# Optimization experiments

Hardware: AMD Instinct MI355X
Metric: run time of the kernel (lower is better)

The kernel has to match this reference:

```python
import jax, jax.numpy as jnp
import numpy as np

N = 50000
E = 800000
D_IN = 128
D_H = 128
N_CLASSES = 40
N_HIDDEN = 2


def _gcn_norm(edge_index, num_nodes):
    # Add self loops, compute symmetric normalization D^-1/2 (A+I) D^-1/2
    loops = jnp.arange(num_nodes, dtype=edge_index.dtype)
    src = jnp.concatenate([edge_index[0], loops])
    dst = jnp.concatenate([edge_index[1], loops])
    deg = jax.ops.segment_sum(jnp.ones_like(src, dtype=jnp.float32), dst,
                              num_segments=num_nodes)
    dinv = jnp.where(deg > 0, jax.lax.rsqrt(jnp.maximum(deg, 1.0)), 0.0)
    norm = dinv[src] * dinv[dst]  # [E+N]
    return src, dst, norm


def _gcn_conv(x, src, dst, norm, W, b):
    h = x @ W                          # [N, d_out] transform first (PyG order)
    msg = h[src] * norm[:, None]       # gather + scale, [E+N, d_out]
    out = jax.ops.segment_sum(msg, dst, num_segments=x.shape[0])
    return out + b


def setup_inputs() -> dict:
    key = jax.random.key(0)
    ks = jax.random.split(key, 8)
    x = jax.random.normal(ks[0], (N, D_IN), dtype=jnp.float32)
    edge_index = jax.random.randint(ks[1], (2, E), 0, N, dtype=jnp.int64)
    s = 1.0 / np.sqrt(D_IN)
    W1 = jax.random.uniform(ks[2], (D_IN, D_H), minval=-s, maxval=s, dtype=jnp.float32)
    b1 = jnp.zeros((D_H,), dtype=jnp.float32)
    sh = 1.0 / np.sqrt(D_H)
    Wh = jax.random.uniform(ks[3], (N_HIDDEN, D_H, D_H), minval=-sh, maxval=sh, dtype=jnp.float32)
    bh = jnp.zeros((N_HIDDEN, D_H), dtype=jnp.float32)
    Wf = jax.random.uniform(ks[4], (D_H, N_CLASSES), minval=-sh, maxval=sh, dtype=jnp.float32)
    bf = jnp.zeros((N_CLASSES,), dtype=jnp.float32)
    return {"x": x, "edge_index": edge_index, "W1": W1, "b1": b1,
            "Wh": Wh, "bh": bh, "Wf": Wf, "bf": bf}


def reference(x, edge_index, W1, b1, Wh, bh, Wf, bf):
    src, dst, norm = _gcn_norm(edge_index, x.shape[0])
    h = jax.nn.relu(_gcn_conv(x, src, dst, norm, W1, b1))
    for i in range(Wh.shape[0]):  # small fixed layer count
        h = jax.nn.relu(_gcn_conv(h, src, dst, norm, Wh[i], bh[i]))
    # extra relu in original forward is a no-op after relu above
    return h @ Wf + bf
```

## Files before the change

### kernel.cpp

```cpp
#include <hip/hip_runtime.h>

#define D 128
#define NC 40

typedef __attribute__((ext_vector_type(8))) short short8v;
typedef __attribute__((ext_vector_type(4))) float f32x4;

__device__ __forceinline__ unsigned short f2bf(float f) {
    unsigned u = __float_as_uint(f);
    u += 0x7fff + ((u >> 16) & 1);
    return (unsigned short)(u >> 16);
}
__device__ __forceinline__ float bf2f(unsigned short h) {
    return __uint_as_float(((unsigned)h) << 16);
}


__global__ void detect_kernel(const int* __restrict__ ei, int* __restrict__ flag) {
    __shared__ int any;
    if (threadIdx.x == 0) any = 0;
    __syncthreads();
    if (ei[threadIdx.x * 2 + 1] != 0) any = 1;
    __syncthreads();
    if (threadIdx.x == 0) *flag = (any == 0) ? 1 : 0;
}

__device__ __forceinline__ int load_idx(const int* ei, long long pos, int is64) {
    return is64 ? ei[pos * 2] : ei[pos];
}

__global__ void count_deg_kernel(const int* __restrict__ ei, const int* __restrict__ flag,
                                 int* __restrict__ deg, int E) {
    int e = blockIdx.x * blockDim.x + threadIdx.x;
    if (e >= E) return;
    int is64 = *flag;
    int d = load_idx(ei, (long long)E + e, is64);
    atomicAdd(&deg[d], 1);
}

__global__ void scan_kernel(const int* __restrict__ deg, int* __restrict__ rowptr,
                            int* __restrict__ fill, float* __restrict__ dinv, int n) {
    __shared__ int wsum[16];
    int t = threadIdx.x;
    int lane = t & 63, w = t >> 6;
    int base = 0;
    int nchunk = (n + 1023) >> 10;
    for (int c = 0; c < nchunk; ++c) {
        int i = (c << 10) + t;
        int v = (i < n) ? deg[i] : 0;
        int s = v;
        #pragma unroll
        for (int off = 1; off < 64; off <<= 1) {
            int x = __shfl_up(s, off, 64);
            if (lane >= off) s += x;
        }
        if (lane == 63) wsum[w] = s;
        __syncthreads();
        int wbase = 0, total = 0;
        #pragma unroll
        for (int j = 0; j < 16; ++j) {
            int ws_j = wsum[j];
            if (j < w) wbase += ws_j;
            total += ws_j;
        }
        int excl = wbase + s - v;
        if (i < n) {
            rowptr[i] = base + excl;
            fill[i]   = base + excl;
            dinv[i]   = rsqrtf((float)(v + 1));
        }
        __syncthreads();
        base += total;
    }
    if (t == 0) rowptr[n] = base;
}

__global__ void scatter_kernel(const int* __restrict__ ei, const int* __restrict__ flag,
                               int* __restrict__ fill, const float* __restrict__ dinv,
                               int2* __restrict__ col2, int E) {
    int e = blockIdx.x * blockDim.x + threadIdx.x;
    if (e >= E) return;
    int is64 = *flag;
    int s = load_idx(ei, (long long)e, is64);
    int d = load_idx(ei, (long long)E + e, is64);
    int pos = atomicAdd(&fill[d], 1);
    col2[pos] = make_int2(s, __float_as_int(dinv[s]));
}

__launch_bounds__(256)
__global__ void gemm128_mfma_kernel(const float* __restrict__ A, const float* __restrict__ W,
                                    float* __restrict__ C, int M) {
    __shared__ unsigned short Ah[64 * 128];
    __shared__ unsigned short Al[64 * 128];
    int t = threadIdx.x;
    int l = t & 63, w = t >> 6;
    int lr = l & 15, lh = l >> 4;

    short8v bhi[2][4], blo[2][4];
    int n0 = w * 32;
    #pragma unroll
    for (int ni = 0; ni < 2; ++ni) {
        #pragma unroll
        for (int ks = 0; ks < 4; ++ks) {
            int n = n0 + ni * 16 + lr;
            int kb = ks * 32 + lh * 8;
            #pragma unroll
            for (int j = 0; j < 8; ++j) {
                float wv = W[(kb + j) * 128 + n];
                unsigned short hi = f2bf(wv);
                unsigned short lo = f2bf(wv - bf2f(hi));
                bhi[ni][ks][j] = (short)hi;
                blo[ni][ks][j] = (short)lo;
            }
        }
    }

    int row0 = blockIdx.x * 64;
    #pragma unroll
    for (int c = 0; c < 4; ++c) {
        int chunk = c * 256 + t;
        int r  = chunk >> 4;
        int kc = chunk & 15;
        int gr = row0 + r; if (gr >= M) gr = M - 1;
        float4 a0 = *(const float4*)&A[(size_t)gr * 128 + kc * 8];
        float4 a1 = *(const float4*)&A[(size_t)gr * 128 + kc * 8 + 4];
        float av[8] = {a0.x, a0.y, a0.z, a0.w, a1.x, a1.y, a1.z, a1.w};
        short8v hv, lv;
        #pragma unroll
        for (int j = 0; j < 8; ++j) {
            unsigned short hi = f2bf(av[j]);
            hv[j] = (short)hi;
            lv[j] = (short)f2bf(av[j] - bf2f(hi));
        }
        int off = (r << 8) + ((kc << 4) ^ ((r & 7) << 4));
        *(short8v*)((char*)Ah + off) = hv;
        *(short8v*)((char*)Al + off) = lv;
    }
    __syncthreads();

    f32x4 acc[4][2];
    #pragma unroll
    for (int mi = 0; mi < 4; ++mi)
        #pragma unroll
        for (int ni = 0; ni < 2; ++ni)
            acc[mi][ni] = (f32x4){0.f, 0.f, 0.f, 0.f};

    #pragma unroll
    for (int mi = 0; mi < 4; ++mi) {
        int row = mi * 16 + lr;
        #pragma unroll
        for (int ks = 0; ks < 4; ++ks) {
            int off = (row << 8) + (((ks << 6) + (lh << 4)) ^ ((row & 7) << 4));
            short8v ah = *(short8v*)((char*)Ah + off);
            short8v al = *(short8v*)((char*)Al + off);
            #pragma unroll
            for (int ni = 0; ni < 2; ++ni) {
                acc[mi][ni] = __builtin_amdgcn_mfma_f32_16x16x32_bf16(ah, bhi[ni][ks], acc[mi][ni], 0, 0, 0);
                acc[mi][ni] = __builtin_amdgcn_mfma_f32_16x16x32_bf16(ah, blo[ni][ks], acc[mi][ni], 0, 0, 0);
                acc[mi][ni] = __builtin_amdgcn_mfma_f32_16x16x32_bf16(al, bhi[ni][ks], acc[mi][ni], 0, 0, 0);
            }
        }
    }

    #pragma unroll
    for (int mi = 0; mi < 4; ++mi) {
        #pragma unroll
        for (int ni = 0; ni < 2; ++ni) {
            #pragma unroll
            for (int r = 0; r < 4; ++r) {
                int row = row0 + mi * 16 + lh * 4 + r;
                if (row < M) C[(size_t)row * 128 + n0 + ni * 16 + lr] = acc[mi][ni][r];
            }
        }
    }
}

__launch_bounds__(256)
__global__ void aggregate_kernel(const float4* __restrict__ h4, const float* __restrict__ dinv,
                                 const int* __restrict__ rowptr, const int2* __restrict__ col2,
                                 const float* __restrict__ bias, float4* __restrict__ out4, int n) {
    int node = blockIdx.x * 8 + (threadIdx.x >> 5);
    if (node >= n) return;
    int l = threadIdx.x & 31;
    float dn = dinv[node];
    size_t rowbase = (size_t)node * 32;
    float4 hv = h4[rowbase + l];
    float4 acc;
    acc.x = hv.x * dn; acc.y = hv.y * dn; acc.z = hv.z * dn; acc.w = hv.w * dn;
    int e = rowptr[node], e1 = rowptr[node + 1];
    for (; e + 8 <= e1; e += 8) {
        int2 c[8];
        #pragma unroll
        for (int j = 0; j < 8; ++j) c[j] = col2[e + j];
        float4 v[8];
        #pragma unroll
        for (int j = 0; j < 8; ++j) v[j] = h4[(size_t)c[j].x * 32 + l];
        #pragma unroll
        for (int j = 0; j < 8; ++j) {
            float ds = __int_as_float(c[j].y);
            acc.x += v[j].x * ds; acc.y += v[j].y * ds;
            acc.z += v[j].z * ds; acc.w += v[j].w * ds;
        }
    }
    for (; e + 4 <= e1; e += 4) {
        int2 c[4];
        #pragma unroll
        for (int j = 0; j < 4; ++j) c[j] = col2[e + j];
        float4 v[4];
        #pragma unroll
        for (int j = 0; j < 4; ++j) v[j] = h4[(size_t)c[j].x * 32 + l];
        #pragma unroll
        for (int j = 0; j < 4; ++j) {
            float ds = __int_as_float(c[j].y);
            acc.x += v[j].x * ds; acc.y += v[j].y * ds;
            acc.z += v[j].z * ds; acc.w += v[j].w * ds;
        }
    }
    for (; e < e1; ++e) {
        int2 c = col2[e];
        float ds = __int_as_float(c.y);
        float4 v = h4[(size_t)c.x * 32 + l];
        acc.x += v.x * ds; acc.y += v.y * ds; acc.z += v.z * ds; acc.w += v.w * ds;
    }
    float4 bv = *(const float4*)&bias[l * 4];
    float4 o;
    o.x = fmaxf(acc.x * dn + bv.x, 0.f);
    o.y = fmaxf(acc.y * dn + bv.y, 0.f);
    o.z = fmaxf(acc.z * dn + bv.z, 0.f);
    o.w = fmaxf(acc.w * dn + bv.w, 0.f);
    out4[rowbase + l] = o;
}

__launch_bounds__(256)
__global__ void final_kernel(const float* __restrict__ A, const float* __restrict__ Wf,
                             const float* __restrict__ bf, float* __restrict__ C, int M) {
    __shared__ float Ws[128 * 40];
    __shared__ float As[64][129];
    int t = threadIdx.x;
    for (int i = t; i < 128 * 40; i += 256) Ws[i] = Wf[i];
    int row0 = blockIdx.x * 64;
    #pragma unroll
    for (int q = 0; q < 8; ++q) {
        int f = q * 256 + t;
        int r = f >> 5;
        int k0 = (f & 31) * 4;
        int gr = row0 + r; if (gr >= M) gr = M - 1;
        float4 av = *(const float4*)&A[(size_t)gr * 128 + k0];
        As[r][k0] = av.x; As[r][k0 + 1] = av.y; As[r][k0 + 2] = av.z; As[r][k0 + 3] = av.w;
    }
    __syncthreads();
    int tx = t & 7, ty = t >> 3;
    int c0 = tx * 5;
    float acc0[5] = {}, acc1[5] = {};
    #pragma unroll 4
    for (int k = 0; k < 128; ++k) {
        float a0 = As[ty][k], a1 = As[ty + 32][k];
        #pragma unroll
        for (int j = 0; j < 5; ++j) {
            float w = Ws[k * 40 + c0 + j];
            acc0[j] += a0 * w;
            acc1[j] += a1 * w;
        }
    }
    int rr0 = row0 + ty, rr1 = row0 + ty + 32;
    #pragma unroll
    for (int j = 0; j < 5; ++j) {
        float b = bf[c0 + j];
        if (rr0 < M) C[(size_t)rr0 * 40 + c0 + j] = acc0[j] + b;
        if (rr1 < M) C[(size_t)rr1 * 40 + c0 + j] = acc1[j] + b;
    }
}

extern "C" void kernel_launch(void* const* d_in, const int* in_sizes, int n_in,
                              void* d_out, int out_size, void* d_ws, size_t ws_size,
                              hipStream_t stream) {
    const float* x  = (const float*)d_in[0];
    const int*   ei = (const int*)d_in[1];
    const float* W1 = (const float*)d_in[2];
    const float* b1 = (const float*)d_in[3];
    const float* Wh = (const float*)d_in[4];
    const float* bh = (const float*)d_in[5];
    const float* Wf = (const float*)d_in[6];
    const float* bf = (const float*)d_in[7];
    float* out = (float*)d_out;

    int n = in_sizes[0] / D;
    int E = in_sizes[1] / 2;

    char* ws = (char*)d_ws;
    size_t off = 0;
    auto alloc = [&](size_t bytes) {
        void* p = ws + off;
        off = (off + bytes + 255) & ~(size_t)255;
        return p;
    };
    float* B0     = (float*)alloc((size_t)n * D * 4);
    float* B1     = (float*)alloc((size_t)n * D * 4);
    int*   deg    = (int*)alloc((size_t)n * 4);
    int*   rowptr = (int*)alloc((size_t)(n + 1) * 4);
    int*   fill   = (int*)alloc((size_t)n * 4);
    int2*  col2   = (int2*)alloc((size_t)E * 8);
    float* dinv   = (float*)alloc((size_t)n * 4);
    int*   flag   = (int*)alloc(256);

    hipMemsetAsync(deg, 0, (size_t)n * 4, stream);
    detect_kernel<<<1, 256, 0, stream>>>(ei, flag);
    count_deg_kernel<<<(E + 255) / 256, 256, 0, stream>>>(ei, flag, deg, E);
    scan_kernel<<<1, 1024, 0, stream>>>(deg, rowptr, fill, dinv, n);
    scatter_kernel<<<(E + 255) / 256, 256, 0, stream>>>(ei, flag, fill, dinv, col2, E);

    int gblocks = (n + 63) / 64;
    int agrid = (n + 7) / 8;

    gemm128_mfma_kernel<<<gblocks, 256, 0, stream>>>(x, W1, B0, n);
    aggregate_kernel<<<agrid, 256, 0, stream>>>((const float4*)B0, dinv, rowptr, col2, b1, (float4*)B1, n);
    gemm128_mfma_kernel<<<gblocks, 256, 0, stream>>>(B1, Wh, B0, n);
    aggregate_kernel<<<agrid, 256, 0, stream>>>((const float4*)B0, dinv, rowptr, col2, bh, (float4*)B1, n);
    gemm128_mfma_kernel<<<gblocks, 256, 0, stream>>>(B1, Wh + D * D, B0, n);
    aggregate_kernel<<<agrid, 256, 0, stream>>>((const float4*)B0, dinv, rowptr, col2, bh + D, (float4*)B1, n);
    final_kernel<<<(n + 63) / 64, 256, 0, stream>>>(B1, Wf, bf, out, n);
}
```

Baseline: 379.8 us.

## Parallelize degree scan, pre-convert weights, pipeline aggregation, MFMA final layer

Replaces the single-block sequential prefix scan with a three-kernel block-parallel scan. Pre-converts each weight matrix once into split bf16 hi/lo transposed buffers so GEMM blocks load ready fragments instead of converting per block. Rewrites the aggregation loop to prefetch the next 8 column entries while gathering the current ones, padding tail entries with zero-weight self entries. Moves the final 128x40 projection onto bf16x3 MFMA. Adds several small kernel launches.

```diff
diff --git a/kernel.cpp b/kernel.cpp
--- a/kernel.cpp
+++ b/kernel.cpp
@@ -38,41 +38,63 @@
     atomicAdd(&deg[d], 1);
 }
 
-__global__ void scan_kernel(const int* __restrict__ deg, int* __restrict__ rowptr,
-                            int* __restrict__ fill, float* __restrict__ dinv, int n) {
-    __shared__ int wsum[16];
+__global__ void scan1_kernel(const int* __restrict__ deg, int* __restrict__ bsum, int n) {
+    int i = blockIdx.x * 256 + threadIdx.x;
+    int v = (i < n) ? deg[i] : 0;
+    #pragma unroll
+    for (int off = 32; off; off >>= 1) v += __shfl_down(v, off, 64);
+    __shared__ int ws[4];
+    if ((threadIdx.x & 63) == 0) ws[threadIdx.x >> 6] = v;
+    __syncthreads();
+    if (threadIdx.x == 0) bsum[blockIdx.x] = ws[0] + ws[1] + ws[2] + ws[3];
+}
+
+__global__ void scan2_kernel(int* __restrict__ bsum, int* __restrict__ total, int nb) {
     int t = threadIdx.x;
     int lane = t & 63, w = t >> 6;
-    int base = 0;
-    int nchunk = (n + 1023) >> 10;
-    for (int c = 0; c < nchunk; ++c) {
-        int i = (c << 10) + t;
-        int v = (i < n) ? deg[i] : 0;
-        int s = v;
-        #pragma unroll
-        for (int off = 1; off < 64; off <<= 1) {
-            int x = __shfl_up(s, off, 64);
-            if (lane >= off) s += x;
-        }
-        if (lane == 63) wsum[w] = s;
-        __syncthreads();
-        int wbase = 0, total = 0;
-        #pragma unroll
-        for (int j = 0; j < 16; ++j) {
-            int ws_j = wsum[j];
-            if (j < w) wbase += ws_j;
-            total += ws_j;
-        }
-        int excl = wbase + s - v;
-        if (i < n) {
-            rowptr[i] = base + excl;
-            fill[i]   = base + excl;
-            dinv[i]   = rsqrtf((float)(v + 1));
-        }
-        __syncthreads();
-        base += total;
-    }
-    if (t == 0) rowptr[n] = base;
+    int v = (t < nb) ? bsum[t] : 0;
+    int s = v;
+    #pragma unroll
+    for (int off = 1; off < 64; off <<= 1) {
+        int x = __shfl_up(s, off, 64);
+        if (lane >= off) s += x;
+    }
+    __shared__ int wsum[16];
+    if (lane == 63) wsum[w] = s;
+    __syncthreads();
+    int wbase = 0;
+    #pragma unroll
+    for (int j = 0; j < 16; ++j) if (j < w) wbase += wsum[j];
+    int excl = wbase + s - v;
+    if (t < nb) bsum[t] = excl;
+    if (t == nb - 1) *total = excl + v;
+}
+
+__global__ void scan3_kernel(const int* __restrict__ deg, const int* __restrict__ bsum,
+                             const int* __restrict__ total, int* __restrict__ rowptr,
+                             int* __restrict__ fill, float* __restrict__ dinv, int n) {
+    int i = blockIdx.x * 256 + threadIdx.x;
+    int v = (i < n) ? deg[i] : 0;
+    int lane = threadIdx.x & 63, w = threadIdx.x >> 6;
+    int s = v;
+    #pragma unroll
+    for (int off = 1; off < 64; off <<= 1) {
+        int x = __shfl_up(s, off, 64);
+        if (lane >= off) s += x;
+    }
+    __shared__ int wsum[4];
+    if (lane == 63) wsum[w] = s;
+    __syncthreads();
+    int wbase = 0;
+    #pragma unroll
+    for (int j = 0; j < 4; ++j) if (j < w) wbase += wsum[j];
+    int excl = bsum[blockIdx.x] + wbase + s - v;
+    if (i < n) {
+        rowptr[i] = excl;
+        fill[i]   = excl;
+        dinv[i]   = rsqrtf((float)(v + 1));
+    }
+    if (i == 0) rowptr[n] = *total;
 }
 
 __global__ void scatter_kernel(const int* __restrict__ ei, const int* __restrict__ flag,
@@ -87,8 +109,19 @@
     col2[pos] = make_int2(s, __float_as_int(dinv[s]));
 }
 
+__global__ void convertW_kernel(const float* __restrict__ W, unsigned short* __restrict__ hi,
+                                unsigned short* __restrict__ lo, int N, int Npad) {
+    int idx = blockIdx.x * blockDim.x + threadIdx.x;
+    if (idx >= Npad * 128) return;
+    int nn = idx >> 7, k = idx & 127;
+    float v = (nn < N) ? W[k * N + nn] : 0.f;
+    unsigned short h = f2bf(v);
+    hi[idx] = h;
+    lo[idx] = f2bf(v - bf2f(h));
+}
+
 __launch_bounds__(256)
-__global__ void gemm128_mfma_kernel(const float* __restrict__ A, const float* __restrict__ W,
+__global__ void gemm128_mfma_kernel(const float* __restrict__ A, const unsigned short* __restrict__ Wcvt,
                                     float* __restrict__ C, int M) {
     __shared__ unsigned short Ah[64 * 128];
     __shared__ unsigned short Al[64 * 128];
@@ -96,22 +129,17 @@
     int l = t & 63, w = t >> 6;
     int lr = l & 15, lh = l >> 4;
 
+    const unsigned short* Whi = Wcvt;
+    const unsigned short* Wlo = Wcvt + 128 * 128;
     short8v bhi[2][4], blo[2][4];
     int n0 = w * 32;
     #pragma unroll
     for (int ni = 0; ni < 2; ++ni) {
+        int n = n0 + ni * 16 + lr;
         #pragma unroll
         for (int ks = 0; ks < 4; ++ks) {
-            int n = n0 + ni * 16 + lr;
-            int kb = ks * 32 + lh * 8;
-            #pragma unroll
-            for (int j = 0; j < 8; ++j) {
-                float wv = W[(kb + j) * 128 + n];
-                unsigned short hi = f2bf(wv);
-                unsigned short lo = f2bf(wv - bf2f(hi));
-                bhi[ni][ks][j] = (short)hi;
-                blo[ni][ks][j] = (short)lo;
-            }
+            bhi[ni][ks] = *(const short8v*)&Whi[n * 128 + ks * 32 + lh * 8];
+            blo[ni][ks] = *(const short8v*)&Wlo[n * 128 + ks * 32 + lh * 8];
         }
     }
 
@@ -188,10 +216,16 @@
     float4 acc;
     acc.x = hv.x * dn; acc.y = hv.y * dn; acc.z = hv.z * dn; acc.w = hv.w * dn;
     int e = rowptr[node], e1 = rowptr[node + 1];
-    for (; e + 8 <= e1; e += 8) {
-        int2 c[8];
-        #pragma unroll
-        for (int j = 0; j < 8; ++j) c[j] = col2[e + j];
+    int2 c[8];
+    #pragma unroll
+    for (int j = 0; j < 8; ++j)
+        c[j] = (e + j < e1) ? col2[e + j] : make_int2(node, 0);
+    while (e < e1) {
+        int en = e + 8;
+        int2 cn[8];
+        #pragma unroll
+        for (int j = 0; j < 8; ++j)
+            cn[j] = (en + j < e1) ? col2[en + j] : make_int2(node, 0);
         float4 v[8];
         #pragma unroll
         for (int j = 0; j < 8; ++j) v[j] = h4[(size_t)c[j].x * 32 + l];
@@ -201,26 +235,9 @@
             acc.x += v[j].x * ds; acc.y += v[j].y * ds;
             acc.z += v[j].z * ds; acc.w += v[j].w * ds;
         }
-    }
-    for (; e + 4 <= e1; e += 4) {
-        int2 c[4];
-        #pragma unroll
-        for (int j = 0; j < 4; ++j) c[j] = col2[e + j];
-        float4 v[4];
-        #pragma unroll
-        for (int j = 0; j < 4; ++j) v[j] = h4[(size_t)c[j].x * 32 + l];
-        #pragma unroll
-        for (int j = 0; j < 4; ++j) {
-            float ds = __int_as_float(c[j].y);
-            acc.x += v[j].x * ds; acc.y += v[j].y * ds;
-            acc.z += v[j].z * ds; acc.w += v[j].w * ds;
-        }
-    }
-    for (; e < e1; ++e) {
-        int2 c = col2[e];
-        float ds = __int_as_float(c.y);
-        float4 v = h4[(size_t)c.x * 32 + l];
-        acc.x += v.x * ds; acc.y += v.y * ds; acc.z += v.z * ds; acc.w += v.w * ds;
+        #pragma unroll
+        for (int j = 0; j < 8; ++j) c[j] = cn[j];
+        e = en;
     }
     float4 bv = *(const float4*)&bias[l * 4];
     float4 o;
@@ -232,42 +249,74 @@
 }
 
 __launch_bounds__(256)
-__global__ void final_kernel(const float* __restrict__ A, const float* __restrict__ Wf,
-                             const float* __restrict__ bf, float* __restrict__ C, int M) {
-    __shared__ float Ws[128 * 40];
-    __shared__ float As[64][129];
+__global__ void final_mfma_kernel(const float* __restrict__ A, const unsigned short* __restrict__ Wcvt,
+                                  const float* __restrict__ bf, float* __restrict__ C, int M) {
+    __shared__ unsigned short Ah[64 * 128];
+    __shared__ unsigned short Al[64 * 128];
     int t = threadIdx.x;
-    for (int i = t; i < 128 * 40; i += 256) Ws[i] = Wf[i];
+    int l = t & 63, w = t >> 6;
+    int lr = l & 15, lh = l >> 4;
+
+    const unsigned short* Whi = Wcvt;
+    const unsigned short* Wlo = Wcvt + 48 * 128;
+    short8v bhi[3][4], blo[3][4];
+    #pragma unroll
+    for (int nt = 0; nt < 3; ++nt) {
+        int n = nt * 16 + lr;
+        #pragma unroll
+        for (int ks = 0; ks < 4; ++ks) {
+            bhi[nt][ks] = *(const short8v*)&Whi[n * 128 + ks * 32 + lh * 8];
+            blo[nt][ks] = *(const short8v*)&Wlo[n * 128 + ks * 32 + lh * 8];
+        }
+    }
+
     int row0 = blockIdx.x * 64;
     #pragma unroll
-    for (int q = 0; q < 8; ++q) {
-        int f = q * 256 + t;
-        int r = f >> 5;
-        int k0 = (f & 31) * 4;
+    for (int c = 0; c < 4; ++c) {
+        int chunk = c * 256 + t;
+        int r  = chunk >> 4;
+        int kc = chunk & 15;
         int gr = row0 + r; if (gr >= M) gr = M - 1;
-        float4 av = *(const float4*)&A[(size_t)gr * 128 + k0];
-        As[r][k0] = av.x; As[r][k0 + 1] = av.y; As[r][k0 + 2] = av.z; As[r][k0 + 3] = av.w;
-    }
-    __syncthreads();
-    int tx = t & 7, ty = t >> 3;
-    int c0 = tx * 5;
-    float acc0[5] = {}, acc1[5] = {};
-    #pragma unroll 4
-    for (int k = 0; k < 128; ++k) {
-        float a0 = As[ty][k], a1 = As[ty + 32][k];
-        #pragma unroll
-        for (int j = 0; j < 5; ++j) {
-            float w = Ws[k * 40 + c0 + j];
-            acc0[j] += a0 * w;
-            acc1[j] += a1 * w;
-        }
-    }
-    int rr0 = row0 + ty, rr1 = row0 + ty + 32;
-    #pragma unroll
-    for (int j = 0; j < 5; ++j) {
-        float b = bf[c0 + j];
-        if (rr0 < M) C[(size_t)rr0 * 40 + c0 + j] = acc0[j] + b;
-        if (rr1 < M) C[(size_t)rr1 * 40 + c0 + j] = acc1[j] + b;
+        float4 a0 = *(const float4*)&A[(size_t)gr * 128 + kc * 8];
+        float4 a1 = *(const float4*)&A[(size_t)gr * 128 + kc * 8 + 4];
+        float av[8] = {a0.x, a0.y, a0.z, a0.w, a1.x, a1.y, a1.z, a1.w};
+        short8v hv, lv;
+        #pragma unroll
+        for (int j = 0; j < 8; ++j) {
+            unsigned short hi = f2bf(av[j]);
+            hv[j] = (short)hi;
+            lv[j] = (short)f2bf(av[j] - bf2f(hi));
+        }
+        int off = (r << 8) + ((kc << 4) ^ ((r & 7) << 4));
+        *(short8v*)((char*)Ah + off) = hv;
+        *(short8v*)((char*)Al + off) = lv;
+    }
+    __syncthreads();
+
+    f32x4 acc[3];
+    #pragma unroll
+    for (int nt = 0; nt < 3; ++nt) acc[nt] = (f32x4){0.f, 0.f, 0.f, 0.f};
+    int row = w * 16 + lr;
+    #pragma unroll
+    for (int ks = 0; ks < 4; ++ks) {
+        int off = (row << 8) + (((ks << 6) + (lh << 4)) ^ ((row & 7) << 4));
+        short8v ah = *(short8v*)((char*)Ah + off);
+        short8v al = *(short8v*)((char*)Al + off);
+        #pragma unroll
+        for (int nt = 0; nt < 3; ++nt) {
+            acc[nt] = __builtin_amdgcn_mfma_f32_16x16x32_bf16(ah, bhi[nt][ks], acc[nt], 0, 0, 0);
+            acc[nt] = __builtin_amdgcn_mfma_f32_16x16x32_bf16(ah, blo[nt][ks], acc[nt], 0, 0, 0);
+            acc[nt] = __builtin_amdgcn_mfma_f32_16x16x32_bf16(al, bhi[nt][ks], acc[nt], 0, 0, 0);
+        }
+    }
+    #pragma unroll
+    for (int nt = 0; nt < 3; ++nt) {
+        int col = nt * 16 + lr;
+        #pragma unroll
+        for (int r = 0; r < 4; ++r) {
+            int ro = row0 + w * 16 + lh * 4 + r;
+            if (col < NC && ro < M) C[(size_t)ro * NC + col] = acc[nt][r] + bf[col];
+        }
     }
 }
 
@@ -302,21 +351,36 @@
     int2*  col2   = (int2*)alloc((size_t)E * 8);
     float* dinv   = (float*)alloc((size_t)n * 4);
     int*   flag   = (int*)alloc(256);
+    int*   bsum   = (int*)alloc(1024 * 4);
+    int*   total  = (int*)alloc(256);
+    unsigned short* Wc1  = (unsigned short*)alloc(2 * 128 * 128 * 2);
+    unsigned short* Wch0 = (unsigned short*)alloc(2 * 128 * 128 * 2);
+    unsigned short* Wch1 = (unsigned short*)alloc(2 * 128 * 128 * 2);
+    unsigned short* Wcf  = (unsigned short*)alloc(2 * 48 * 128 * 2);
+
+    int nb = (n + 255) / 256;
 
     hipMemsetAsync(deg, 0, (size_t)n * 4, stream);
     detect_kernel<<<1, 256, 0, stream>>>(ei, flag);
     count_deg_kernel<<<(E + 255) / 256, 256, 0, stream>>>(ei, flag, deg, E);
-    scan_kernel<<<1, 1024, 0, stream>>>(deg, rowptr, fill, dinv, n);
+    scan1_kernel<<<nb, 256, 0, stream>>>(deg, bsum, n);
+    scan2_kernel<<<1, 1024, 0, stream>>>(bsum, total, nb);
+    scan3_kernel<<<nb, 256, 0, stream>>>(deg, bsum, total, rowptr, fill, dinv, n);
     scatter_kernel<<<(E + 255) / 256, 256, 0, stream>>>(ei, flag, fill, dinv, col2, E);
+
+    convertW_kernel<<<(128 * 128 + 255) / 256, 256, 0, stream>>>(W1, Wc1, Wc1 + 128 * 128, 128, 128);
+    convertW_kernel<<<(128 * 128 + 255) / 256, 256, 0, stream>>>(Wh, Wch0, Wch0 + 128 * 128, 128, 128);
+    convertW_kernel<<<(128 * 128 + 255) / 256, 256, 0, stream>>>(Wh + 128 * 128, Wch1, Wch1 + 128 * 128, 128, 128);
+    convertW_kernel<<<(48 * 128 + 255) / 256, 256, 0, stream>>>(Wf, Wcf, Wcf + 48 * 128, 40, 48);
 
     int gblocks = (n + 63) / 64;
     int agrid = (n + 7) / 8;
 
-    gemm128_mfma_kernel<<<gblocks, 256, 0, stream>>>(x, W1, B0, n);
+    gemm128_mfma_kernel<<<gblocks, 256, 0, stream>>>(x, Wc1, B0, n);
     aggregate_kernel<<<agrid, 256, 0, stream>>>((const float4*)B0, dinv, rowptr, col2, b1, (float4*)B1, n);
-    gemm128_mfma_kernel<<<gblocks, 256, 0, stream>>>(B1, Wh, B0, n);
+    gemm128_mfma_kernel<<<gblocks, 256, 0, stream>>>(B1, Wch0, B0, n);
     aggregate_kernel<<<agrid, 256, 0, stream>>>((const float4*)B0, dinv, rowptr, col2, bh, (float4*)B1, n);
-    gemm128_mfma_kernel<<<gblocks, 256, 0, stream>>>(B1, Wh + D * D, B0, n);
+    gemm128_mfma_kernel<<<gblocks, 256, 0, stream>>>(B1, Wch1, B0, n);
     aggregate_kernel<<<agrid, 256, 0, stream>>>((const float4*)B0, dinv, rowptr, col2, bh + D, (float4*)B1, n);
-    final_kernel<<<(n + 63) / 64, 256, 0, stream>>>(B1, Wf, bf, out, n);
-}
+    final_mfma_kernel<<<gblocks, 256, 0, stream>>>(B1, Wcf, bf, out, n);
+}
```

After: 355.3 us. 6.4% less time.
